# Kernel optimization log

Measured on AMD Instinct MI355X. Metric: run time of the kernel, lower is better.

Reference implementation:

```python
import jax, jax.numpy as jnp
import numpy as np

N, M, E0, E1, D, C_IN, NCLS = 100000, 10000, 1600000, 320000, 64, 4, 4


def setup_inputs() -> dict:
    key = jax.random.key(0)
    ks = jax.random.split(key, 16)
    w = lambda k, shp: jax.random.normal(k, shp, jnp.float32) * 0.05
    return {
        "features": jax.random.normal(ks[0], (N, C_IN), jnp.float32),
        "points": jax.random.uniform(ks[1], (N, 3), dtype=jnp.float32),
        "cluster_centers": jax.random.uniform(ks[2], (M, 3), dtype=jnp.float32),
        "labels": jax.random.randint(ks[3], (N,), 0, M, jnp.int32),
        "l0_edges": jax.random.randint(ks[4], (E0, 2), 0, N, jnp.int32),
        "l1_edges": jax.random.randint(ks[5], (E1, 2), 0, M, jnp.int32),
        "fe_W": w(ks[6], (C_IN + 3, D)), "fe_b": jnp.zeros((D,), jnp.float32),
        "gnn_Wh": w(ks[7], (3, D, 3)), "gnn_bh": jnp.zeros((3, 3), jnp.float32),
        "gnn_Wf": w(ks[8], (3, D + 3, D)), "gnn_bf": jnp.zeros((3, D), jnp.float32),
        "gnn_Wg": w(ks[9], (3, D, D)), "gnn_bg": jnp.zeros((3, D), jnp.float32),
        "m2l_W": w(ks[10], (D + 3, D)), "m2l_b": jnp.zeros((D,), jnp.float32),
        "l2m_W": w(ks[11], (D + 3, D)), "l2m_b": jnp.zeros((D,), jnp.float32),
        "cls_W1": w(ks[12], (D, D)), "cls_b1": jnp.zeros((D,), jnp.float32),
        "cls_W2": w(ks[13], (D, NCLS)), "cls_b2": jnp.zeros((NCLS,), jnp.float32),
    }


def _seg_max(x, idx, n):
    # unsorted segment max; empty segments -> 0 (TF scatter_max-with-floor style)
    agg = jax.ops.segment_max(x, idx, num_segments=n)
    return jnp.where(agg <= jnp.finfo(x.dtype).min * 0.5, 0.0, agg)


def _pointgnn_layer(x, pos, edges, Wh, bh, Wf, bf, Wg, bg):
    # PointGNN layer: offset MLP, edge MLP on gathered (rel_pos+offset, src feat),
    # scatter-max to destination, update MLP, residual.
    delta = jnp.tanh(x @ Wh + bh)                     # [n,3] learned coord offset
    s, d = edges[:, 0], edges[:, 1]
    rel = pos[s] - pos[d] + delta[d]                  # [E,3]
    e = jax.nn.relu(jnp.concatenate([rel, x[s]], -1) @ Wf + bf)  # [E,D]
    agg = _seg_max(e, d, x.shape[0])                  # [n,D]
    return jax.nn.relu(agg @ Wg + bg) + x


def _forward(features, points, cluster_centers, labels, l0_edges, l1_edges,
             fe_W, fe_b, gnn_Wh, gnn_bh, gnn_Wf, gnn_bf, gnn_Wg, gnn_bg,
             m2l_W, m2l_b, l2m_W, l2m_b, cls_W1, cls_b1, cls_W2, cls_b2):
    rel = points - cluster_centers[labels]            # [N,3] point rel to its center
    # layer1: Feature_extract
    x1 = jax.nn.relu(jnp.concatenate([features, rel], -1) @ fe_W + fe_b)
    # layer2: Mini_GNN on point graph
    x2 = _pointgnn_layer(x1, points, l0_edges, gnn_Wh[0], gnn_bh[0],
                         gnn_Wf[0], gnn_bf[0], gnn_Wg[0], gnn_bg[0])
    # layer3: Mini_to_Large (scatter-max pooling to clusters)
    h = jax.nn.relu(jnp.concatenate([x2, rel], -1) @ m2l_W + m2l_b)
    c = _seg_max(h, labels, cluster_centers.shape[0])  # [M,D]
    # layer4: GNN on cluster graph
    c4 = _pointgnn_layer(c, cluster_centers, l1_edges, gnn_Wh[1], gnn_bh[1],
                         gnn_Wf[1], gnn_bf[1], gnn_Wg[1], gnn_bg[1])
    # layer5: Large_to_Mini (broadcast cluster features back to points)
    x5 = jax.nn.relu(jnp.concatenate([c4[labels], rel], -1) @ l2m_W + l2m_b)
    # layer6: Mini_GNN on point graph
    x6 = _pointgnn_layer(x5, points, l0_edges, gnn_Wh[2], gnn_bh[2],
                         gnn_Wf[2], gnn_bf[2], gnn_Wg[2], gnn_bg[2])
    final = x6 + x2                                   # residual skip per source
    return jax.nn.relu(final @ cls_W1 + cls_b1) @ cls_W2 + cls_b2  # [N,NCLS]


def reference(features, points, cluster_centers, labels, l0_edges, l1_edges,
              fe_W, fe_b, gnn_Wh, gnn_bh, gnn_Wf, gnn_bf, gnn_Wg, gnn_bg,
              m2l_W, m2l_b, l2m_W, l2m_b, cls_W1, cls_b1, cls_W2, cls_b2):
    return _forward(features, points, cluster_centers, labels, l0_edges, l1_edges,
                    fe_W, fe_b, gnn_Wh, gnn_bh, gnn_Wf, gnn_bf, gnn_Wg, gnn_bg,
                    m2l_W, m2l_b, l2m_W, l2m_b, cls_W1, cls_b1, cls_W2, cls_b2)
```

## Files before the change

kernel.cpp:

```cpp
#include <hip/hip_runtime.h>


__device__ __forceinline__ float bcast(float v, int l) {
    return __int_as_float(__builtin_amdgcn_readlane(__float_as_int(v), l));
}

#define REPD(M,P,B) \
 M(0,P,B)  M(1,P,B)  M(2,P,B)  M(3,P,B)  M(4,P,B)  M(5,P,B)  M(6,P,B)  M(7,P,B) \
 M(8,P,B)  M(9,P,B)  M(10,P,B) M(11,P,B) M(12,P,B) M(13,P,B) M(14,P,B) M(15,P,B) \
 M(16,P,B) M(17,P,B) M(18,P,B) M(19,P,B) M(20,P,B) M(21,P,B) M(22,P,B) M(23,P,B) \
 M(24,P,B) M(25,P,B) M(26,P,B) M(27,P,B) M(28,P,B) M(29,P,B) M(30,P,B) M(31,P,B) \
 M(32,P,B) M(33,P,B) M(34,P,B) M(35,P,B) M(36,P,B) M(37,P,B) M(38,P,B) M(39,P,B) \
 M(40,P,B) M(41,P,B) M(42,P,B) M(43,P,B) M(44,P,B) M(45,P,B) M(46,P,B) M(47,P,B) \
 M(48,P,B) M(49,P,B) M(50,P,B) M(51,P,B) M(52,P,B) M(53,P,B) M(54,P,B) M(55,P,B) \
 M(56,P,B) M(57,P,B) M(58,P,B) M(59,P,B) M(60,P,B) M(61,P,B) M(62,P,B) M(63,P,B)

#define WLOAD(J,P,B) float P##J = (B)[(J)*64+lane];

#define REPP(M,P,X,S0,S1) \
 M(0,1,P,X,S0,S1)  M(2,3,P,X,S0,S1)  M(4,5,P,X,S0,S1)  M(6,7,P,X,S0,S1) \
 M(8,9,P,X,S0,S1)  M(10,11,P,X,S0,S1) M(12,13,P,X,S0,S1) M(14,15,P,X,S0,S1) \
 M(16,17,P,X,S0,S1) M(18,19,P,X,S0,S1) M(20,21,P,X,S0,S1) M(22,23,P,X,S0,S1) \
 M(24,25,P,X,S0,S1) M(26,27,P,X,S0,S1) M(28,29,P,X,S0,S1) M(30,31,P,X,S0,S1) \
 M(32,33,P,X,S0,S1) M(34,35,P,X,S0,S1) M(36,37,P,X,S0,S1) M(38,39,P,X,S0,S1) \
 M(40,41,P,X,S0,S1) M(42,43,P,X,S0,S1) M(44,45,P,X,S0,S1) M(46,47,P,X,S0,S1) \
 M(48,49,P,X,S0,S1) M(50,51,P,X,S0,S1) M(52,53,P,X,S0,S1) M(54,55,P,X,S0,S1) \
 M(56,57,P,X,S0,S1) M(58,59,P,X,S0,S1) M(60,61,P,X,S0,S1) M(62,63,P,X,S0,S1)

#define WFMA(J,K,P,X,S0,S1) \
 S0 = fmaf(bcast(X,J), P##J, S0); \
 S1 = fmaf(bcast(X,K), P##K, S1);


typedef short bf16x8 __attribute__((ext_vector_type(8)));
typedef float f32x4  __attribute__((ext_vector_type(4)));

__device__ __forceinline__ unsigned short f2bf_rne(float x) {
    unsigned u = __float_as_uint(x);
    unsigned r = u + 0x7FFFu + ((u >> 16) & 1u);
    return (unsigned short)(r >> 16);
}

__device__ __forceinline__ void a_frag(const float* __restrict__ row, int kt, int g4,
                                       bf16x8& ah, bf16x8& al)
{
    const float4 a0 = *(const float4*)(row + kt*32 + g4);
    const float4 a1 = *(const float4*)(row + kt*32 + 16 + g4);
    float v0 = a0.x, v1 = a0.y, v2 = a0.z, v3 = a0.w;
    float v4 = a1.x, v5 = a1.y, v6 = a1.z, v7 = a1.w;
#define CVT1(idx, val) { \
    unsigned short hh = f2bf_rne(val); \
    float lf = (val) - __uint_as_float((unsigned)hh << 16); \
    ah[idx] = (short)hh; al[idx] = (short)f2bf_rne(lf); }
    CVT1(0,v0) CVT1(1,v1) CVT1(2,v2) CVT1(3,v3)
    CVT1(4,v4) CVT1(5,v5) CVT1(6,v6) CVT1(7,v7)
#undef CVT1
}

__device__ __forceinline__ void mm64(const bf16x8& ah0, const bf16x8& al0,
                                     const bf16x8& ah1, const bf16x8& al1,
                                     const unsigned short* __restrict__ pW,
                                     int lane, f32x4 acc[4])
{
#pragma unroll
    for (int nt = 0; nt < 4; ++nt) {
        f32x4 a = {0.f, 0.f, 0.f, 0.f};
#pragma unroll
        for (int kt = 0; kt < 2; ++kt) {
            bf16x8 bh = *(const bf16x8*)(pW + (kt*4+nt)*1024 + lane*8);
            bf16x8 bl = *(const bf16x8*)(pW + (kt*4+nt)*1024 + 512 + lane*8);
            bf16x8 aH = kt ? ah1 : ah0;
            bf16x8 aL = kt ? al1 : al0;
            a = __builtin_amdgcn_mfma_f32_16x16x32_bf16(aH, bh, a, 0, 0, 0);
            a = __builtin_amdgcn_mfma_f32_16x16x32_bf16(aL, bh, a, 0, 0, 0);
            a = __builtin_amdgcn_mfma_f32_16x16x32_bf16(aH, bl, a, 0, 0, 0);
        }
        acc[nt] = a;
    }
}

__global__ __launch_bounds__(256) void k_packB7(
    const float* W0, unsigned short* d0, const float* W1, unsigned short* d1,
    const float* W2, unsigned short* d2, const float* W3, unsigned short* d3,
    const float* W4, unsigned short* d4, const float* W5, unsigned short* d5,
    const float* W6, unsigned short* d6)
{
    const float* W; unsigned short* dst;
    switch (blockIdx.x) {
        case 0: W=W0; dst=d0; break;
        case 1: W=W1; dst=d1; break;
        case 2: W=W2; dst=d2; break;
        case 3: W=W3; dst=d3; break;
        case 4: W=W4; dst=d4; break;
        case 5: W=W5; dst=d5; break;
        default: W=W6; dst=d6; break;
    }
    int t = threadIdx.x;
    for (int slot = t; slot < 512; slot += 256) {
        int frag = slot >> 6;
        int lane = slot & 63;
        int kt = frag >> 2, nt = frag & 3;
        int g4 = (lane >> 4) * 4, n = nt*16 + (lane & 15);
        for (int j = 0; j < 8; ++j) {
            int k = kt*32 + (j>>2)*16 + g4 + (j&3);
            float x = W[k*64 + n];
            unsigned short hh = f2bf_rne(x);
            float lf = x - __uint_as_float((unsigned)hh << 16);
            dst[frag*1024 + 0*512 + lane*8 + j] = hh;
            dst[frag*1024 + 1*512 + lane*8 + j] = f2bf_rne(lf);
        }
    }
}


__global__ __launch_bounds__(256) void k_zero3(
    int* c0, int n0, int* c1, int n1, int* c2, int n2)
{
    int t = threadIdx.x;
    for (int i = t; i < n0; i += 256) c0[i] = 0;
    for (int i = t; i < n1; i += 256) c1[i] = 0;
    for (int i = t; i < n2; i += 256) c2[i] = 0;
}

__global__ __launch_bounds__(256) void k_bhist3(
    const int2* __restrict__ e0, int* cnt0, int E0, int nb0,
    const int2* __restrict__ e1, int* cnt1, int E1, int nb1,
    const int* __restrict__ lab, int* cntL, int NN, int nbL)
{
    const int2* e = nullptr; const int* lv = nullptr; int* gcnt; int total; int nb;
    int bloc, nblocks;
    int b = blockIdx.x;
    if (b < 1024)      { e = e0; gcnt = cnt0; total = E0; nb = nb0; bloc = b;        nblocks = 1024; }
    else if (b < 1280) { e = e1; gcnt = cnt1; total = E1; nb = nb1; bloc = b - 1024; nblocks = 256; }
    else               { lv = lab; gcnt = cntL; total = NN; nb = nbL; bloc = b - 1280; nblocks = 256; }
    __shared__ int c[400];
    for (int i = threadIdx.x; i < nb; i += 256) c[i] = 0;
    __syncthreads();
    for (int idx = bloc*256 + threadIdx.x; idx < total; idx += nblocks*256)
        atomicAdd(&c[(lv ? lv[idx] : e[idx].y) >> 8], 1);
    __syncthreads();
    for (int i = threadIdx.x; i < nb; i += 256) if (c[i]) atomicAdd(&gcnt[i], c[i]);
}

__global__ __launch_bounds__(512) void k_bscan3(
    const int* c0, int* b0, int* u0, int nb0, int t0,
    const int* c1, int* b1, int* u1, int nb1, int t1,
    const int* c2, int* b2, int* u2, int nb2, int t2)
{
    const int* cnt; int* base; int* cur; int nb; int tot;
    if (blockIdx.x == 0) { cnt=c0; base=b0; cur=u0; nb=nb0; tot=t0; }
    else if (blockIdx.x == 1) { cnt=c1; base=b1; cur=u1; nb=nb1; tot=t1; }
    else { cnt=c2; base=b2; cur=u2; nb=nb2; tot=t2; }
    __shared__ int sc[512];
    int t = threadIdx.x;
    int v = (t < nb) ? cnt[t] : 0;
    sc[t] = v; __syncthreads();
    for (int o = 1; o < 512; o <<= 1) {
        int a = (t >= o) ? sc[t-o] : 0;
        __syncthreads();
        sc[t] += a;
        __syncthreads();
    }
    if (t < nb) { int ex = sc[t] - v; base[t] = ex; cur[t] = ex; }
    if (t == nb) base[nb] = tot;
}

#define BKT 512
#define EPT 8
#define EPB (BKT*EPT)
__global__ __launch_bounds__(BKT) void k_bucket3(
    const int2* __restrict__ e0, int* cur0, int2* eb0, int E0, int nb0, int GB0,
    const int2* __restrict__ e1, int* cur1, int2* eb1, int E1, int nb1, int GB1,
    const int* __restrict__ lab, int* curL, int2* ebL, int NN, int nbL)
{
    const int2* e = nullptr; const int* lv = nullptr; int* cur; int2* ebuf;
    int total; int nb; int bloc;
    int b = blockIdx.x;
    if (b < GB0)            { e = e0; cur = cur0; ebuf = eb0; total = E0; nb = nb0; bloc = b; }
    else if (b < GB0 + GB1) { e = e1; cur = cur1; ebuf = eb1; total = E1; nb = nb1; bloc = b - GB0; }
    else                    { lv = lab; cur = curL; ebuf = ebL; total = NN; nb = nbL; bloc = b - GB0 - GB1; }
    __shared__ int cnt[400];
    __shared__ int chunk[400];
    int t = threadIdx.x;
    int base = bloc * EPB;
    for (int i = t; i < nb; i += BKT) cnt[i] = 0;
    __syncthreads();
    int2 ed[EPT]; int rk[EPT];
#pragma unroll
    for (int k = 0; k < EPT; ++k) {
        int idx = base + k*BKT + t;
        if (idx < total) {
            ed[k] = lv ? make_int2(idx, lv[idx]) : e[idx];
            rk[k] = atomicAdd(&cnt[ed[k].y >> 8], 1);
        } else rk[k] = -1;
    }
    __syncthreads();
    for (int i = t; i < nb; i += BKT) { int c = cnt[i]; if (c) chunk[i] = atomicAdd(&cur[i], c); }
    __syncthreads();
#pragma unroll
    for (int k = 0; k < EPT; ++k)
        if (rk[k] >= 0) ebuf[chunk[ed[k].y >> 8] + rk[k]] = ed[k];
}

__global__ __launch_bounds__(512) void k_final3(
    const int2* eb0, const int* base0, int* rs0, int* srcs0, int nd0, int et0, int NB0_,
    const int2* eb1, const int* base1, int* rs1, int* srcs1, int nd1, int et1, int NB1_,
    const int2* ebL, const int* baseL, int* rsL, int* srcsL, int ndL, int etL, int NBL_)
{
    const int2* ebuf; const int* base_; int* rs; int* srcs; int ndst; int etot; int nb; int bloc;
    int b = blockIdx.x;
    if (b < NB0_)              { ebuf=eb0; base_=base0; rs=rs0; srcs=srcs0; ndst=nd0; etot=et0; nb=NB0_; bloc=b; }
    else if (b < NB0_ + NB1_)  { ebuf=eb1; base_=base1; rs=rs1; srcs=srcs1; ndst=nd1; etot=et1; nb=NB1_; bloc=b-NB0_; }
    else                       { ebuf=ebL; base_=baseL; rs=rsL; srcs=srcsL; ndst=ndL; etot=etL; nb=NBL_; bloc=b-NB0_-NB1_; }
    __shared__ int h[256];
    __shared__ int sc[256];
    int t = threadIdx.x;
    int base = base_[bloc];
    int cnt  = base_[bloc+1] - base;
    int d0 = bloc << 8;
    if (t < 256) h[t] = 0;
    __syncthreads();
    for (int i = t; i < cnt; i += 512) atomicAdd(&h[ebuf[base+i].y - d0], 1);
    __syncthreads();
    int v = (t < 256) ? h[t] : 0;
    if (t < 256) sc[t] = v;
    __syncthreads();
    for (int o = 1; o < 256; o <<= 1) {
        int a = (t < 256 && t >= o) ? sc[t-o] : 0;
        __syncthreads();
        if (t < 256) sc[t] += a;
        __syncthreads();
    }
    if (t < 256) {
        int gpos = base + sc[t] - v;
        if (d0 + t < ndst) rs[d0+t] = gpos;
        h[t] = gpos;
    }
    if (bloc == nb-1 && t == 0) rs[ndst] = etot;
    __syncthreads();
    for (int i = t; i < cnt; i += 512) {
        int2 ed = ebuf[base+i];
        int pos = atomicAdd(&h[ed.y - d0], 1);
        srcs[pos] = ed.x;
    }
}


__global__ __launch_bounds__(256) void k_feat_pre0_g(
    const float* __restrict__ feat, const float* __restrict__ pts,
    const float* __restrict__ ctr, const int* __restrict__ lab,
    const float* __restrict__ Wfe, const float* __restrict__ bfe,
    const float* __restrict__ Wh, const float* __restrict__ bh,
    const unsigned short* __restrict__ pWf0, const float* __restrict__ Wf0h,
    const float* __restrict__ bf0,
    float* __restrict__ rel, float* __restrict__ x1,
    float* __restrict__ p, float* __restrict__ q, int ntiles)
{
    __shared__ float xp[4][16*68];
    __shared__ float dd[4][64];
    int lane = threadIdx.x & 63;
    int w = threadIdx.x >> 6;
    int tile = blockIdx.x*4 + w;
    if (tile >= ntiles) return;
    int r0 = tile*16;
    int row = lane & 15;
    int cg  = lane >> 4;
    int r = r0 + row;
    int l = lab[r];
    float pr0 = pts[r*3+0], pr1 = pts[r*3+1], pr2 = pts[r*3+2];
    float rv0 = pr0 - ctr[l*3+0], rv1 = pr1 - ctr[l*3+1], rv2 = pr2 - ctr[l*3+2];
    if (cg == 0) { rel[r*3+0]=rv0; rel[r*3+1]=rv1; rel[r*3+2]=rv2; }
    float f0 = feat[r*4+0], f1 = feat[r*4+1], f2 = feat[r*4+2], f3 = feat[r*4+3];
#pragma unroll
    for (int k = 0; k < 16; ++k) {
        int c = cg*16 + k;
        float v = bfe[c];
        v = fmaf(f0, Wfe[0*64+c], v);
        v = fmaf(f1, Wfe[1*64+c], v);
        v = fmaf(f2, Wfe[2*64+c], v);
        v = fmaf(f3, Wfe[3*64+c], v);
        v = fmaf(rv0, Wfe[4*64+c], v);
        v = fmaf(rv1, Wfe[5*64+c], v);
        v = fmaf(rv2, Wfe[6*64+c], v);
        xp[w][row*68 + c] = fmaxf(v, 0.f);
    }
    {
        int j = cg < 3 ? cg : 2;
        float accd = 0.f;
#pragma unroll 16
        for (int k2 = 0; k2 < 64; ++k2)
            accd = fmaf(xp[w][row*68 + k2], Wh[k2*3 + j], accd);
        dd[w][row*4 + cg] = tanhf(accd + bh[j]);
    }
    int g4 = cg * 4;
    const float* lrow = &xp[w][row*68];
    bf16x8 ah0, al0, ah1, al1;
    a_frag(lrow, 0, g4, ah0, al0);
    a_frag(lrow, 1, g4, ah1, al1);
    f32x4 acc[4];
    mm64(ah0, al0, ah1, al1, pWf0, lane, acc);
    int rloc = cg*4;
#pragma unroll
    for (int nt = 0; nt < 4; ++nt) {
        int c = nt*16 + row;
        float w0t = Wf0h[0*64+c], w1t = Wf0h[1*64+c], w2t = Wf0h[2*64+c];
        float bfc = bf0[c];
#pragma unroll
        for (int reg = 0; reg < 4; ++reg) {
            int rr = r0 + rloc + reg;
            int rl = rloc + reg;
            float pp0 = pts[rr*3+0], pp1 = pts[rr*3+1], pp2 = pts[rr*3+2];
            float v = acc[nt][reg] + pp0*w0t + pp1*w1t + pp2*w2t;
            p[(size_t)rr*64 + c] = v;
            x1[(size_t)rr*64 + c] = xp[w][rl*68 + c];
            float d0 = dd[w][rl*4+0], d1 = dd[w][rl*4+1], d2 = dd[w][rl*4+2];
            q[(size_t)rr*64 + c] = (d0-pp0)*w0t + (d1-pp1)*w1t + (d2-pp2)*w2t + bfc;
        }
    }
}

__global__ __launch_bounds__(256) void k_post_m2l_g(
    const float* __restrict__ agg, const unsigned short* __restrict__ pWg,
    const float* __restrict__ bg, const float* __restrict__ x1,
    const unsigned short* __restrict__ pWm, const float* __restrict__ bm,
    const float* __restrict__ Wmt, const float* __restrict__ rel,
    float* __restrict__ x2, float* __restrict__ h, int ntiles)
{
    __shared__ float xp[4][16*68];
    int lane = threadIdx.x & 63;
    int w = threadIdx.x >> 6;
    int tile = blockIdx.x*4 + w;
    if (tile >= ntiles) return;
    int r0 = tile*16;
    int g4 = (lane >> 4) * 4;
    int rloc = (lane >> 4) * 4;
    const float* rowp = agg + (size_t)(r0 + (lane & 15)) * 64;
    bf16x8 ah0, al0, ah1, al1;
    a_frag(rowp, 0, g4, ah0, al0);
    a_frag(rowp, 1, g4, ah1, al1);
    f32x4 acc[4];
    mm64(ah0, al0, ah1, al1, pWg, lane, acc);
#pragma unroll
    for (int nt = 0; nt < 4; ++nt) {
        int c = nt*16 + (lane & 15);
        float bc = bg[c];
#pragma unroll
        for (int reg = 0; reg < 4; ++reg) {
            int r = r0 + rloc + reg;
            float v = fmaxf(acc[nt][reg] + bc, 0.f) + x1[(size_t)r*64 + c];
            x2[(size_t)r*64 + c] = v;
            xp[w][(rloc+reg)*68 + c] = v;
        }
    }
    const float* lrow = &xp[w][(lane & 15)*68];
    a_frag(lrow, 0, g4, ah0, al0);
    a_frag(lrow, 1, g4, ah1, al1);
    mm64(ah0, al0, ah1, al1, pWm, lane, acc);
#pragma unroll
    for (int nt = 0; nt < 4; ++nt) {
        int c = nt*16 + (lane & 15);
        float bc = bm[c];
        float w0t = Wmt[0*64+c], w1t = Wmt[1*64+c], w2t = Wmt[2*64+c];
#pragma unroll
        for (int reg = 0; reg < 4; ++reg) {
            int r = r0 + rloc + reg;
            float v = acc[nt][reg] + bc + rel[r*3+0]*w0t + rel[r*3+1]*w1t + rel[r*3+2]*w2t;
            h[(size_t)r*64 + c] = fmaxf(v, 0.f);
        }
    }
}

__global__ __launch_bounds__(256) void k_l2m_pre2_g(
    const float* __restrict__ c4, const int* __restrict__ lab,
    const unsigned short* __restrict__ pWl, const float* __restrict__ bl,
    const float* __restrict__ Wlt, const float* __restrict__ rel,
    const unsigned short* __restrict__ pWf2, const float* __restrict__ Wf2t,
    const float* __restrict__ pts,
    const float* __restrict__ Wh, const float* __restrict__ bh,
    const float* __restrict__ bf,
    float* __restrict__ x5, float* __restrict__ p, float* __restrict__ q, int ntiles)
{
    __shared__ float xp[4][16*68];
    __shared__ float dd[4][64];
    int lane = threadIdx.x & 63;
    int w = threadIdx.x >> 6;
    int tile = blockIdx.x*4 + w;
    if (tile >= ntiles) return;
    int r0 = tile*16;
    int g4 = (lane >> 4) * 4;
    int rloc = (lane >> 4) * 4;
    int rA = r0 + (lane & 15);
    const float* rowp = c4 + (size_t)lab[rA] * 64;
    bf16x8 ah0, al0, ah1, al1;
    a_frag(rowp, 0, g4, ah0, al0);
    a_frag(rowp, 1, g4, ah1, al1);
    f32x4 acc[4];
    mm64(ah0, al0, ah1, al1, pWl, lane, acc);
#pragma unroll
    for (int nt = 0; nt < 4; ++nt) {
        int c = nt*16 + (lane & 15);
        float bc = bl[c];
        float w0t = Wlt[0*64+c], w1t = Wlt[1*64+c], w2t = Wlt[2*64+c];
#pragma unroll
        for (int reg = 0; reg < 4; ++reg) {
            int r = r0 + rloc + reg;
            float v = acc[nt][reg] + bc + rel[r*3+0]*w0t + rel[r*3+1]*w1t + rel[r*3+2]*w2t;
            v = fmaxf(v, 0.f);
            x5[(size_t)r*64 + c] = v;
            xp[w][(rloc+reg)*68 + c] = v;
        }
    }
    {
        int rowl = lane & 15;
        int jj = lane >> 4;
        int j = jj < 3 ? jj : 2;
        float accd = 0.f;
#pragma unroll 16
        for (int k = 0; k < 64; ++k)
            accd = fmaf(xp[w][rowl*68 + k], Wh[k*3 + j], accd);
        dd[w][rowl*4 + jj] = tanhf(accd + bh[j]);
    }
    const float* lrow = &xp[w][(lane & 15)*68];
    a_frag(lrow, 0, g4, ah0, al0);
    a_frag(lrow, 1, g4, ah1, al1);
    mm64(ah0, al0, ah1, al1, pWf2, lane, acc);
#pragma unroll
    for (int nt = 0; nt < 4; ++nt) {
        int c = nt*16 + (lane & 15);
        float w0t = Wf2t[0*64+c], w1t = Wf2t[1*64+c], w2t = Wf2t[2*64+c];
        float bfc = bf[c];
#pragma unroll
        for (int reg = 0; reg < 4; ++reg) {
            int r = r0 + rloc + reg;
            int rl = rloc + reg;
            float p0 = pts[r*3+0], p1 = pts[r*3+1], p2 = pts[r*3+2];
            float v = acc[nt][reg] + p0*w0t + p1*w1t + p2*w2t;
            p[(size_t)r*64 + c] = v;
            float d0 = dd[w][rl*4+0], d1 = dd[w][rl*4+1], d2 = dd[w][rl*4+2];
            q[(size_t)r*64 + c] = (d0-p0)*w0t + (d1-p1)*w1t + (d2-p2)*w2t + bfc;
        }
    }
}

__global__ __launch_bounds__(256) void k_gemm_final(
    const float* __restrict__ agg, const unsigned short* __restrict__ pWg2,
    const float* __restrict__ bg2,
    const float* __restrict__ x5, const float* __restrict__ x2,
    const unsigned short* __restrict__ pW1, const float* __restrict__ b1,
    const float* __restrict__ W2, const float* __restrict__ b2,
    float* __restrict__ out, int ntiles)
{
    __shared__ float xp[4][16*68];
    int lane = threadIdx.x & 63;
    int w = threadIdx.x >> 6;
    int tile = blockIdx.x*4 + w;
    if (tile >= ntiles) return;
    int r0 = tile*16;
    int g4 = (lane >> 4) * 4;
    int rloc = (lane >> 4) * 4;
    const float* rowp = agg + (size_t)(r0 + (lane & 15)) * 64;
    bf16x8 ah0, al0, ah1, al1;
    a_frag(rowp, 0, g4, ah0, al0);
    a_frag(rowp, 1, g4, ah1, al1);
    f32x4 acc[4];
    mm64(ah0, al0, ah1, al1, pWg2, lane, acc);
#pragma unroll
    for (int nt = 0; nt < 4; ++nt) {
        int c = nt*16 + (lane & 15);
        float bc = bg2[c];
#pragma unroll
        for (int reg = 0; reg < 4; ++reg) {
            int r = r0 + rloc + reg;
            float v = fmaxf(acc[nt][reg] + bc, 0.f)
                    + x5[(size_t)r*64 + c] + x2[(size_t)r*64 + c];
            xp[w][(rloc+reg)*68 + c] = v;
        }
    }
    const float* lrow = &xp[w][(lane & 15)*68];
    a_frag(lrow, 0, g4, ah0, al0);
    a_frag(lrow, 1, g4, ah1, al1);
    mm64(ah0, al0, ah1, al1, pW1, lane, acc);
    float part0[4] = {0.f,0.f,0.f,0.f};
    float part1[4] = {0.f,0.f,0.f,0.f};
    float part2[4] = {0.f,0.f,0.f,0.f};
    float part3[4] = {0.f,0.f,0.f,0.f};
#pragma unroll
    for (int nt = 0; nt < 4; ++nt) {
        int c = nt*16 + (lane & 15);
        float bc = b1[c];
        float4 w2v = *(const float4*)(W2 + c*4);
#pragma unroll
        for (int reg = 0; reg < 4; ++reg) {
            float t = fmaxf(acc[nt][reg] + bc, 0.f);
            part0[reg] = fmaf(t, w2v.x, part0[reg]);
            part1[reg] = fmaf(t, w2v.y, part1[reg]);
            part2[reg] = fmaf(t, w2v.z, part2[reg]);
            part3[reg] = fmaf(t, w2v.w, part3[reg]);
        }
    }
#pragma unroll
    for (int m = 1; m < 16; m <<= 1) {
#pragma unroll
        for (int reg = 0; reg < 4; ++reg) {
            part0[reg] += __shfl_xor(part0[reg], m);
            part1[reg] += __shfl_xor(part1[reg], m);
            part2[reg] += __shfl_xor(part2[reg], m);
            part3[reg] += __shfl_xor(part3[reg], m);
        }
    }
    if ((lane & 15) == 0) {
        float b20 = b2[0], b21 = b2[1], b22 = b2[2], b23 = b2[3];
#pragma unroll
        for (int reg = 0; reg < 4; ++reg) {
            int r = r0 + rloc + reg;
            *(float4*)(out + (size_t)r*4) =
                make_float4(part0[reg]+b20, part1[reg]+b21, part2[reg]+b22, part3[reg]+b23);
        }
    }
}


__global__ __launch_bounds__(256) void k_seg_max_gnn(
    const int* __restrict__ rs, const int* __restrict__ srcs,
    const float* __restrict__ p, float* __restrict__ q, int n)
{
    int lane = threadIdx.x & 63;
    int wid  = blockIdx.x * (blockDim.x >> 6) + (threadIdx.x >> 6);
    int nw   = gridDim.x * (blockDim.x >> 6);
    for (int d0 = wid*2; d0 < n; d0 += nw*2) {
        int dA = __builtin_amdgcn_readfirstlane(d0);
        int begA = rs[dA], endA = rs[dA+1], endB = rs[dA+2];
        int ca = begA, cb = endA;
        float aA[8], aB[8];
#pragma unroll
        for (int u = 0; u < 8; ++u) { aA[u] = -1e30f; aB[u] = -1e30f; }
        while (ca+8 <= endA && cb+8 <= endB) {
            int sA[8], sB[8];
#pragma unroll
            for (int u = 0; u < 8; ++u) { sA[u] = srcs[ca+u]; sB[u] = srcs[cb+u]; }
#pragma unroll
            for (int u = 0; u < 8; ++u) {
                aA[u] = fmaxf(aA[u], p[(size_t)sA[u]*64+lane]);
                aB[u] = fmaxf(aB[u], p[(size_t)sB[u]*64+lane]);
            }
            ca += 8; cb += 8;
        }
        while (ca+4 <= endA) {
            int s0=srcs[ca], s1=srcs[ca+1], s2=srcs[ca+2], s3=srcs[ca+3];
            aA[0] = fmaxf(aA[0], p[(size_t)s0*64+lane]);
            aA[1] = fmaxf(aA[1], p[(size_t)s1*64+lane]);
            aA[2] = fmaxf(aA[2], p[(size_t)s2*64+lane]);
            aA[3] = fmaxf(aA[3], p[(size_t)s3*64+lane]);
            ca += 4;
        }
        while (cb+4 <= endB) {
            int t0=srcs[cb], t1=srcs[cb+1], t2=srcs[cb+2], t3=srcs[cb+3];
            aB[0] = fmaxf(aB[0], p[(size_t)t0*64+lane]);
            aB[1] = fmaxf(aB[1], p[(size_t)t1*64+lane]);
            aB[2] = fmaxf(aB[2], p[(size_t)t2*64+lane]);
            aB[3] = fmaxf(aB[3], p[(size_t)t3*64+lane]);
            cb += 4;
        }
        while (ca+2 <= endA) {
            int s0=srcs[ca], s1=srcs[ca+1];
            aA[0] = fmaxf(aA[0], p[(size_t)s0*64+lane]);
            aA[1] = fmaxf(aA[1], p[(size_t)s1*64+lane]);
            ca += 2;
        }
        while (cb+2 <= endB) {
            int t0=srcs[cb], t1=srcs[cb+1];
            aB[0] = fmaxf(aB[0], p[(size_t)t0*64+lane]);
            aB[1] = fmaxf(aB[1], p[(size_t)t1*64+lane]);
            cb += 2;
        }
        if (ca < endA) aA[0] = fmaxf(aA[0], p[(size_t)srcs[ca]*64+lane]);
        if (cb < endB) aB[0] = fmaxf(aB[0], p[(size_t)srcs[cb]*64+lane]);
        float accA = fmaxf(fmaxf(fmaxf(aA[0],aA[1]), fmaxf(aA[2],aA[3])),
                           fmaxf(fmaxf(aA[4],aA[5]), fmaxf(aA[6],aA[7])));
        float accB = fmaxf(fmaxf(fmaxf(aB[0],aB[1]), fmaxf(aB[2],aB[3])),
                           fmaxf(fmaxf(aB[4],aB[5]), fmaxf(aB[6],aB[7])));
        size_t oA = (size_t)dA*64 + lane, oB = oA + 64;
        q[oA] = fmaxf(accA + q[oA], 0.f);
        q[oB] = fmaxf(accB + q[oB], 0.f);
    }
}

__global__ __launch_bounds__(256, 2) void k_seglab_pre1(
    const int* __restrict__ rsL, const int* __restrict__ srcsL,
    const float* __restrict__ h, const float* __restrict__ pos,
    const float* __restrict__ Wh, const float* __restrict__ bh,
    const float* __restrict__ Wf, const float* __restrict__ bf,
    float* __restrict__ c, float* __restrict__ pa, float* __restrict__ qa, int m)
{
    int lane = threadIdx.x & 63;
    int wid  = blockIdx.x * (blockDim.x >> 6) + (threadIdx.x >> 6);
    int nw   = gridDim.x * (blockDim.x >> 6);
    REPD(WLOAD, wc, Wf + 3*64)
    float w0 = Wf[0*64+lane], w1 = Wf[1*64+lane], w2 = Wf[2*64+lane];
    float bfl = bf[lane];
    float wh0 = Wh[lane*3+0], wh1 = Wh[lane*3+1], wh2 = Wh[lane*3+2];
    float bh0 = bh[0], bh1 = bh[1], bh2 = bh[2];
    for (int d0 = wid*2; d0 < m; d0 += nw*2) {
        int dA = __builtin_amdgcn_readfirstlane(d0);
        int dB = dA + 1;
        int begA = rsL[dA], endA = rsL[dA+1], endB = rsL[dA+2];
        int ca = begA, cb = endA;
        float aA0=-1e30f, aA1=-1e30f, aB0=-1e30f, aB1=-1e30f;
        while (ca+2 <= endA && cb+2 <= endB) {
            int s0=srcsL[ca], s1=srcsL[ca+1], s2=srcsL[cb], s3=srcsL[cb+1];
            aA0 = fmaxf(aA0, h[(size_t)s0*64+lane]);
            aA1 = fmaxf(aA1, h[(size_t)s1*64+lane]);
            aB0 = fmaxf(aB0, h[(size_t)s2*64+lane]);
            aB1 = fmaxf(aB1, h[(size_t)s3*64+lane]);
            ca += 2; cb += 2;
        }
        while (ca+2 <= endA) {
            int s0=srcsL[ca], s1=srcsL[ca+1];
            aA0 = fmaxf(aA0, h[(size_t)s0*64+lane]);
            aA1 = fmaxf(aA1, h[(size_t)s1*64+lane]);
            ca += 2;
        }
        while (cb+2 <= endB) {
            int s2=srcsL[cb], s3=srcsL[cb+1];
            aB0 = fmaxf(aB0, h[(size_t)s2*64+lane]);
            aB1 = fmaxf(aB1, h[(size_t)s3*64+lane]);
            cb += 2;
        }
        if (ca < endA) aA0 = fmaxf(aA0, h[(size_t)srcsL[ca]*64+lane]);
        if (cb < endB) aB0 = fmaxf(aB0, h[(size_t)srcsL[cb]*64+lane]);
        float cvA = fmaxf(fmaxf(aA0,aA1), 0.f);
        float cvB = fmaxf(fmaxf(aB0,aB1), 0.f);
        c[(size_t)dA*64+lane] = cvA;
        c[(size_t)dB*64+lane] = cvB;
        float d0A = cvA*wh0, d1A = cvA*wh1, d2A = cvA*wh2;
        float d0B = cvB*wh0, d1B = cvB*wh1, d2B = cvB*wh2;
#pragma unroll
        for (int o = 32; o; o >>= 1) {
            d0A += __shfl_xor(d0A,o); d1A += __shfl_xor(d1A,o); d2A += __shfl_xor(d2A,o);
            d0B += __shfl_xor(d0B,o); d1B += __shfl_xor(d1B,o); d2B += __shfl_xor(d2B,o);
        }
        d0A = tanhf(d0A+bh0); d1A = tanhf(d1A+bh1); d2A = tanhf(d2A+bh2);
        d0B = tanhf(d0B+bh0); d1B = tanhf(d1B+bh1); d2B = tanhf(d2B+bh2);
        float pA0 = pos[dA*3+0], pA1 = pos[dA*3+1], pA2 = pos[dA*3+2];
        float pB0 = pos[dB*3+0], pB1 = pos[dB*3+1], pB2 = pos[dB*3+2];
        float s0A=0.f, s1A=0.f, s0B=0.f, s1B=0.f;
        REPP(WFMA, wc, cvA, s0A, s1A)
        REPP(WFMA, wc, cvB, s0B, s1B)
        pa[(size_t)dA*64+lane] = s0A+s1A + pA0*w0 + pA1*w1 + pA2*w2;
        pa[(size_t)dB*64+lane] = s0B+s1B + pB0*w0 + pB1*w1 + pB2*w2;
        qa[(size_t)dA*64+lane] = (d0A-pA0)*w0 + (d1A-pA1)*w1 + (d2A-pA2)*w2 + bfl;
        qa[(size_t)dB*64+lane] = (d0B-pB0)*w0 + (d1B-pB1)*w1 + (d2B-pB2)*w2 + bfl;
    }
}

__global__ __launch_bounds__(256, 2) void k_gnn_post(
    const float* __restrict__ agg, const float* __restrict__ Wg,
    const float* __restrict__ bg, const float* __restrict__ xres,
    float* __restrict__ out, int n)
{
    int lane = threadIdx.x & 63;
    int wid  = blockIdx.x * (blockDim.x >> 6) + (threadIdx.x >> 6);
    int nw   = gridDim.x * (blockDim.x >> 6);
    REPD(WLOAD, wg, Wg)
    float bgl = bg[lane];
    for (int i0 = wid*2; i0 < n; i0 += nw*2) {
        int iA = __builtin_amdgcn_readfirstlane(i0);
        size_t oA = (size_t)iA*64 + lane, oB = oA + 64;
        float avA = agg[oA], avB = agg[oB];
        float s0A=0.f, s1A=0.f, s0B=0.f, s1B=0.f;
        REPP(WFMA, wg, avA, s0A, s1A)
        REPP(WFMA, wg, avB, s0B, s1B)
        out[oA] = fmaxf(s0A+s1A + bgl, 0.f) + xres[oA];
        out[oB] = fmaxf(s0B+s1B + bgl, 0.f) + xres[oB];
    }
}


extern "C" void kernel_launch(void* const* d_in, const int* in_sizes, int n_in,
                              void* d_out, int out_size, void* d_ws, size_t ws_size,
                              hipStream_t stream)
{
    const int N = 100000, M = 10000, E0 = 1600000, E1 = 320000;
    const int NB0 = (N + 255) / 256;
    const int NB1 = (M + 255) / 256;
    const int NBL = (M + 255) / 256;
    const int GB0 = (E0 + EPB - 1) / EPB;
    const int GB1 = (E1 + EPB - 1) / EPB;
    const int GBL = (N + EPB - 1) / EPB;

    const float* feat = (const float*)d_in[0];
    const float* pts  = (const float*)d_in[1];
    const float* ctr  = (const float*)d_in[2];
    const int*   lab  = (const int*)d_in[3];
    const int2*  e0   = (const int2*)d_in[4];
    const int2*  e1   = (const int2*)d_in[5];
    const float* feW  = (const float*)d_in[6];
    const float* feb  = (const float*)d_in[7];
    const float* Wh   = (const float*)d_in[8];
    const float* bh   = (const float*)d_in[9];
    const float* Wf   = (const float*)d_in[10];
    const float* bf   = (const float*)d_in[11];
    const float* Wg   = (const float*)d_in[12];
    const float* bg   = (const float*)d_in[13];
    const float* m2lW = (const float*)d_in[14];
    const float* m2lb = (const float*)d_in[15];
    const float* l2mW = (const float*)d_in[16];
    const float* l2mb = (const float*)d_in[17];
    const float* cW1  = (const float*)d_in[18];
    const float* cb1  = (const float*)d_in[19];
    const float* cW2  = (const float*)d_in[20];
    const float* cb2  = (const float*)d_in[21];
    float* out = (float*)d_out;

    char* ws = (char*)d_ws;
    size_t off = 0;
    auto alloc = [&](size_t bytes) -> char* {
        char* r = ws + off; off += (bytes + 255) & ~(size_t)255; return r;
    };
    float* rel   = (float*)alloc((size_t)N*3*4);
    float* x1    = (float*)alloc((size_t)N*64*4);
    float* x2    = (float*)alloc((size_t)N*64*4);
    float* p     = (float*)alloc((size_t)N*64*4);
    float* q     = (float*)alloc((size_t)N*64*4);
    float* c     = (float*)alloc((size_t)M*64*4);
    float* c4    = (float*)alloc((size_t)M*64*4);
    int* rs0     = (int*)alloc((size_t)(N+2)*4);
    int* srcs0   = (int*)alloc((size_t)E0*4);
    int* rs1     = (int*)alloc((size_t)(M+2)*4);
    int* srcs1   = (int*)alloc((size_t)E1*4);
    int* rsL     = (int*)alloc((size_t)(M+2)*4);
    int* srcsL   = (int*)alloc((size_t)N*4);
    int* cnt0    = (int*)alloc((size_t)NB0*4);
    int* cnt1    = (int*)alloc((size_t)NB1*4);
    int* cntL    = (int*)alloc((size_t)NBL*4);
    int* base0   = (int*)alloc((size_t)(NB0+1)*4);
    int* base1   = (int*)alloc((size_t)(NB1+1)*4);
    int* baseL   = (int*)alloc((size_t)(NBL+1)*4);
    int* cur0    = (int*)alloc((size_t)NB0*4);
    int* cur1    = (int*)alloc((size_t)NB1*4);
    int* curL    = (int*)alloc((size_t)NBL*4);
    unsigned short* pWf0  = (unsigned short*)alloc(8192*2);
    unsigned short* pWg0  = (unsigned short*)alloc(8192*2);
    unsigned short* pWm   = (unsigned short*)alloc(8192*2);
    unsigned short* pWl2m = (unsigned short*)alloc(8192*2);
    unsigned short* pWf2  = (unsigned short*)alloc(8192*2);
    unsigned short* pWg2  = (unsigned short*)alloc(8192*2);
    unsigned short* pW1   = (unsigned short*)alloc(8192*2);
    (void)ws_size; (void)in_sizes; (void)n_in; (void)out_size;

    int2* ebuf0 = (int2*)x2;
    int2* ebuf1 = ebuf0 + E0;
    int2* ebufL = ebuf1 + E1;

    dim3 blk(256);
    const int gridM = 640, gSeg = 3072;
    const int NT = N / 16;
    const int gG = (NT + 3) / 4;

    k_packB7<<<7, blk, 0, stream>>>(
        Wf + 0*67*64 + 3*64, pWf0,
        Wg + 0*64*64,        pWg0,
        m2lW,                pWm,
        l2mW,                pWl2m,
        Wf + 2*67*64 + 3*64, pWf2,
        Wg + 2*64*64,        pWg2,
        cW1,                 pW1);

    k_zero3<<<1, blk, 0, stream>>>(cnt0, NB0, cnt1, NB1, cntL, NBL);
    k_bhist3<<<1536, blk, 0, stream>>>(e0, cnt0, E0, NB0,
                                       e1, cnt1, E1, NB1,
                                       lab, cntL, N, NBL);
    k_bscan3<<<3, 512, 0, stream>>>(cnt0, base0, cur0, NB0, E0,
                                    cnt1, base1, cur1, NB1, E1,
                                    cntL, baseL, curL, NBL, N);
    k_bucket3<<<GB0 + GB1 + GBL, BKT, 0, stream>>>(
        e0, cur0, ebuf0, E0, NB0, GB0,
        e1, cur1, ebuf1, E1, NB1, GB1,
        lab, curL, ebufL, N, NBL);
    k_final3<<<NB0 + NB1 + NBL, 512, 0, stream>>>(
        ebuf0, base0, rs0, srcs0, N, E0, NB0,
        ebuf1, base1, rs1, srcs1, M, E1, NB1,
        ebufL, baseL, rsL, srcsL, M, N, NBL);

    k_feat_pre0_g<<<gG, blk, 0, stream>>>(feat, pts, ctr, lab, feW, feb,
                                          Wh+0*64*3, bh+0*3,
                                          pWf0, Wf+0*67*64, bf+0*64,
                                          rel, x1, p, q, NT);
    k_seg_max_gnn<<<gSeg, blk, 0, stream>>>(rs0, srcs0, p, q, N);
    k_post_m2l_g<<<gG, blk, 0, stream>>>(q, pWg0, bg+0*64, x1,
                                         pWm, m2lb, m2lW+64*64, rel,
                                         x2, p, NT);

    float* p1 = q;
    float* q1 = q + (size_t)M*64;
    k_seglab_pre1<<<gridM, blk, 0, stream>>>(rsL, srcsL, p, ctr,
                                             Wh+1*64*3, bh+1*3, Wf+1*67*64, bf+1*64,
                                             c, p1, q1, M);
    k_seg_max_gnn<<<640, blk, 0, stream>>>(rs1, srcs1, p1, q1, M);
    k_gnn_post<<<gridM, blk, 0, stream>>>(q1, Wg+1*64*64, bg+1*64, c, c4, M);

    k_l2m_pre2_g<<<gG, blk, 0, stream>>>(c4, lab, pWl2m, l2mb, l2mW+64*64, rel,
                                         pWf2, Wf+2*67*64, pts,
                                         Wh+2*64*3, bh+2*3, bf+2*64,
                                         x1, p, q, NT);
    k_seg_max_gnn<<<gSeg, blk, 0, stream>>>(rs0, srcs0, p, q, N);
    k_gemm_final<<<gG, blk, 0, stream>>>(q, pWg2, bg+2*64, x1, x2,
                                         pW1, cb1, cW2, cb2, out, NT);
}
```

Measured before the change: 333.4 us.

## Fuse weight packing with histogram kernel and rewrite segment-max gather as float2 half-waves

The weight-packing kernel and the edge/label histogram kernel are merged into one launch, which removes one kernel launch. The seg-max kernel now handles one destination per wave instead of two. Each half-wave gathers alternating source rows with float2 loads, and the two halves are combined with a cross-lane shuffle. The aim is wider per-lane loads and more independent gathers in flight, at the cost of an extra shuffle. The seg-max grid also shrinks from 3072 to 2048 blocks.

```diff
diff --git a/kernel.cpp b/kernel.cpp
--- a/kernel.cpp
+++ b/kernel.cpp
@@ -79,39 +79,66 @@
     }
 }
 
-__global__ __launch_bounds__(256) void k_packB7(
+
+#define BKT 512
+#define EPT 8
+#define EPB (BKT*EPT)
+
+__global__ __launch_bounds__(256) void k_prep(
     const float* W0, unsigned short* d0, const float* W1, unsigned short* d1,
     const float* W2, unsigned short* d2, const float* W3, unsigned short* d3,
     const float* W4, unsigned short* d4, const float* W5, unsigned short* d5,
-    const float* W6, unsigned short* d6)
-{
-    const float* W; unsigned short* dst;
-    switch (blockIdx.x) {
-        case 0: W=W0; dst=d0; break;
-        case 1: W=W1; dst=d1; break;
-        case 2: W=W2; dst=d2; break;
-        case 3: W=W3; dst=d3; break;
-        case 4: W=W4; dst=d4; break;
-        case 5: W=W5; dst=d5; break;
-        default: W=W6; dst=d6; break;
-    }
-    int t = threadIdx.x;
-    for (int slot = t; slot < 512; slot += 256) {
-        int frag = slot >> 6;
-        int lane = slot & 63;
-        int kt = frag >> 2, nt = frag & 3;
-        int g4 = (lane >> 4) * 4, n = nt*16 + (lane & 15);
-        for (int j = 0; j < 8; ++j) {
-            int k = kt*32 + (j>>2)*16 + g4 + (j&3);
-            float x = W[k*64 + n];
-            unsigned short hh = f2bf_rne(x);
-            float lf = x - __uint_as_float((unsigned)hh << 16);
-            dst[frag*1024 + 0*512 + lane*8 + j] = hh;
-            dst[frag*1024 + 1*512 + lane*8 + j] = f2bf_rne(lf);
-        }
-    }
-}
-
+    const float* W6, unsigned short* d6,
+    int* cnt0, int nb0, int* cnt1, int nb1, int* cntL, int nbL,
+    const int2* __restrict__ e0, int E0,
+    const int2* __restrict__ e1, int E1,
+    const int* __restrict__ lab, int NN)
+{
+    int b = blockIdx.x;
+    if (b < 7) {
+        const float* W; unsigned short* dst;
+        switch (b) {
+            case 0: W=W0; dst=d0; break;
+            case 1: W=W1; dst=d1; break;
+            case 2: W=W2; dst=d2; break;
+            case 3: W=W3; dst=d3; break;
+            case 4: W=W4; dst=d4; break;
+            case 5: W=W5; dst=d5; break;
+            default: W=W6; dst=d6; break;
+        }
+        int t = threadIdx.x;
+        for (int slot = t; slot < 512; slot += 256) {
+            int frag = slot >> 6;
+            int lane = slot & 63;
+            int kt = frag >> 2, nt = frag & 3;
+            int g4 = (lane >> 4) * 4, n = nt*16 + (lane & 15);
+            for (int j = 0; j < 8; ++j) {
+                int k = kt*32 + (j>>2)*16 + g4 + (j&3);
+                float x = W[k*64 + n];
+                unsigned short hh = f2bf_rne(x);
+                float lf = x - __uint_as_float((unsigned)hh << 16);
+                dst[frag*1024 + 0*512 + lane*8 + j] = hh;
+                dst[frag*1024 + 1*512 + lane*8 + j] = f2bf_rne(lf);
+            }
+        }
+        return;
+    }
+    {
+        const int2* e = nullptr; const int* lv = nullptr; int* gcnt; int total; int nb;
+        int bloc, nblocks;
+        int bb = b - 7;
+        if (bb < 1024)      { e = e0; gcnt = cnt0; total = E0; nb = nb0; bloc = bb;        nblocks = 1024; }
+        else if (bb < 1280) { e = e1; gcnt = cnt1; total = E1; nb = nb1; bloc = bb - 1024; nblocks = 256; }
+        else                { lv = lab; gcnt = cntL; total = NN; nb = nbL; bloc = bb - 1280; nblocks = 256; }
+        __shared__ int c[400];
+        for (int i = threadIdx.x; i < nb; i += 256) c[i] = 0;
+        __syncthreads();
+        for (int idx = bloc*256 + threadIdx.x; idx < total; idx += nblocks*256)
+            atomicAdd(&c[(lv ? lv[idx] : e[idx].y) >> 8], 1);
+        __syncthreads();
+        for (int i = threadIdx.x; i < nb; i += 256) if (c[i]) atomicAdd(&gcnt[i], c[i]);
+    }
+}
 
 __global__ __launch_bounds__(256) void k_zero3(
     int* c0, int n0, int* c1, int n1, int* c2, int n2)
@@ -120,26 +147,6 @@
     for (int i = t; i < n0; i += 256) c0[i] = 0;
     for (int i = t; i < n1; i += 256) c1[i] = 0;
     for (int i = t; i < n2; i += 256) c2[i] = 0;
-}
-
-__global__ __launch_bounds__(256) void k_bhist3(
-    const int2* __restrict__ e0, int* cnt0, int E0, int nb0,
-    const int2* __restrict__ e1, int* cnt1, int E1, int nb1,
-    const int* __restrict__ lab, int* cntL, int NN, int nbL)
-{
-    const int2* e = nullptr; const int* lv = nullptr; int* gcnt; int total; int nb;
-    int bloc, nblocks;
-    int b = blockIdx.x;
-    if (b < 1024)      { e = e0; gcnt = cnt0; total = E0; nb = nb0; bloc = b;        nblocks = 1024; }
-    else if (b < 1280) { e = e1; gcnt = cnt1; total = E1; nb = nb1; bloc = b - 1024; nblocks = 256; }
-    else               { lv = lab; gcnt = cntL; total = NN; nb = nbL; bloc = b - 1280; nblocks = 256; }
-    __shared__ int c[400];
-    for (int i = threadIdx.x; i < nb; i += 256) c[i] = 0;
-    __syncthreads();
-    for (int idx = bloc*256 + threadIdx.x; idx < total; idx += nblocks*256)
-        atomicAdd(&c[(lv ? lv[idx] : e[idx].y) >> 8], 1);
-    __syncthreads();
-    for (int i = threadIdx.x; i < nb; i += 256) if (c[i]) atomicAdd(&gcnt[i], c[i]);
 }
 
 __global__ __launch_bounds__(512) void k_bscan3(
@@ -165,9 +172,6 @@
     if (t == nb) base[nb] = tot;
 }
 
-#define BKT 512
-#define EPT 8
-#define EPB (BKT*EPT)
 __global__ __launch_bounds__(BKT) void k_bucket3(
     const int2* __restrict__ e0, int* cur0, int2* eb0, int E0, int nb0, int GB0,
     const int2* __restrict__ e1, int* cur1, int2* eb1, int E1, int nb1, int GB1,
@@ -525,63 +529,68 @@
     const float* __restrict__ p, float* __restrict__ q, int n)
 {
     int lane = threadIdx.x & 63;
+    int half = lane >> 5;
+    int cl   = lane & 31;
     int wid  = blockIdx.x * (blockDim.x >> 6) + (threadIdx.x >> 6);
     int nw   = gridDim.x * (blockDim.x >> 6);
-    for (int d0 = wid*2; d0 < n; d0 += nw*2) {
-        int dA = __builtin_amdgcn_readfirstlane(d0);
-        int begA = rs[dA], endA = rs[dA+1], endB = rs[dA+2];
-        int ca = begA, cb = endA;
-        float aA[8], aB[8];
-#pragma unroll
-        for (int u = 0; u < 8; ++u) { aA[u] = -1e30f; aB[u] = -1e30f; }
-        while (ca+8 <= endA && cb+8 <= endB) {
-            int sA[8], sB[8];
-#pragma unroll
-            for (int u = 0; u < 8; ++u) { sA[u] = srcs[ca+u]; sB[u] = srcs[cb+u]; }
+    const float2* p2 = (const float2*)p;
+    for (int d = wid; d < n; d += nw) {
+        int du = __builtin_amdgcn_readfirstlane(d);
+        int beg = rs[du], end = rs[du+1];
+        float ax[8], ay[8];
+#pragma unroll
+        for (int u = 0; u < 8; ++u) { ax[u] = -1e30f; ay[u] = -1e30f; }
+        int c = beg;
+        while (c + 16 <= end) {
+            int s[8];
+#pragma unroll
+            for (int u = 0; u < 8; ++u) s[u] = srcs[c + 2*u + half];
 #pragma unroll
             for (int u = 0; u < 8; ++u) {
-                aA[u] = fmaxf(aA[u], p[(size_t)sA[u]*64+lane]);
-                aB[u] = fmaxf(aB[u], p[(size_t)sB[u]*64+lane]);
+                float2 v = p2[(size_t)s[u]*32 + cl];
+                ax[u] = fmaxf(ax[u], v.x);
+                ay[u] = fmaxf(ay[u], v.y);
             }
-            ca += 8; cb += 8;
-        }
-        while (ca+4 <= endA) {
-            int s0=srcs[ca], s1=srcs[ca+1], s2=srcs[ca+2], s3=srcs[ca+3];
-            aA[0] = fmaxf(aA[0], p[(size_t)s0*64+lane]);
-            aA[1] = fmaxf(aA[1], p[(size_t)s1*64+lane]);
-            aA[2] = fmaxf(aA[2], p[(size_t)s2*64+lane]);
-            aA[3] = fmaxf(aA[3], p[(size_t)s3*64+lane]);
-            ca += 4;
-        }
-        while (cb+4 <= endB) {
-            int t0=srcs[cb], t1=srcs[cb+1], t2=srcs[cb+2], t3=srcs[cb+3];
-            aB[0] = fmaxf(aB[0], p[(size_t)t0*64+lane]);
-            aB[1] = fmaxf(aB[1], p[(size_t)t1*64+lane]);
-            aB[2] = fmaxf(aB[2], p[(size_t)t2*64+lane]);
-            aB[3] = fmaxf(aB[3], p[(size_t)t3*64+lane]);
-            cb += 4;
-        }
-        while (ca+2 <= endA) {
-            int s0=srcs[ca], s1=srcs[ca+1];
-            aA[0] = fmaxf(aA[0], p[(size_t)s0*64+lane]);
-            aA[1] = fmaxf(aA[1], p[(size_t)s1*64+lane]);
-            ca += 2;
-        }
-        while (cb+2 <= endB) {
-            int t0=srcs[cb], t1=srcs[cb+1];
-            aB[0] = fmaxf(aB[0], p[(size_t)t0*64+lane]);
-            aB[1] = fmaxf(aB[1], p[(size_t)t1*64+lane]);
-            cb += 2;
-        }
-        if (ca < endA) aA[0] = fmaxf(aA[0], p[(size_t)srcs[ca]*64+lane]);
-        if (cb < endB) aB[0] = fmaxf(aB[0], p[(size_t)srcs[cb]*64+lane]);
-        float accA = fmaxf(fmaxf(fmaxf(aA[0],aA[1]), fmaxf(aA[2],aA[3])),
-                           fmaxf(fmaxf(aA[4],aA[5]), fmaxf(aA[6],aA[7])));
-        float accB = fmaxf(fmaxf(fmaxf(aB[0],aB[1]), fmaxf(aB[2],aB[3])),
-                           fmaxf(fmaxf(aB[4],aB[5]), fmaxf(aB[6],aB[7])));
-        size_t oA = (size_t)dA*64 + lane, oB = oA + 64;
-        q[oA] = fmaxf(accA + q[oA], 0.f);
-        q[oB] = fmaxf(accB + q[oB], 0.f);
+            c += 16;
+        }
+        while (c + 8 <= end) {
+            int s0 = srcs[c + half],     s1 = srcs[c + 2 + half];
+            int s2 = srcs[c + 4 + half], s3 = srcs[c + 6 + half];
+            float2 v0 = p2[(size_t)s0*32 + cl];
+            float2 v1 = p2[(size_t)s1*32 + cl];
+            float2 v2 = p2[(size_t)s2*32 + cl];
+            float2 v3 = p2[(size_t)s3*32 + cl];
+            ax[0] = fmaxf(ax[0], v0.x); ay[0] = fmaxf(ay[0], v0.y);
+            ax[1] = fmaxf(ax[1], v1.x); ay[1] = fmaxf(ay[1], v1.y);
+            ax[2] = fmaxf(ax[2], v2.x); ay[2] = fmaxf(ay[2], v2.y);
+            ax[3] = fmaxf(ax[3], v3.x); ay[3] = fmaxf(ay[3], v3.y);
+            c += 8;
+        }
+        while (c + 2 <= end) {
+            int s0 = srcs[c + half];
+            float2 v = p2[(size_t)s0*32 + cl];
+            ax[0] = fmaxf(ax[0], v.x);
+            ay[0] = fmaxf(ay[0], v.y);
+            c += 2;
+        }
+        if (c < end) {
+            int s0 = srcs[c];
+            float2 v = p2[(size_t)s0*32 + cl];
+            ax[0] = fmaxf(ax[0], v.x);
+            ay[0] = fmaxf(ay[0], v.y);
+        }
+        float mx = fmaxf(fmaxf(fmaxf(ax[0],ax[1]), fmaxf(ax[2],ax[3])),
+                         fmaxf(fmaxf(ax[4],ax[5]), fmaxf(ax[6],ax[7])));
+        float my = fmaxf(fmaxf(fmaxf(ay[0],ay[1]), fmaxf(ay[2],ay[3])),
+                         fmaxf(fmaxf(ay[4],ay[5]), fmaxf(ay[6],ay[7])));
+        mx = fmaxf(mx, __shfl_xor(mx, 32));
+        my = fmaxf(my, __shfl_xor(my, 32));
+        if (half == 0) {
+            float2* q2 = (float2*)q;
+            size_t o = (size_t)du*32 + cl;
+            float2 qv = q2[o];
+            q2[o] = make_float2(fmaxf(mx + qv.x, 0.f), fmaxf(my + qv.y, 0.f));
+        }
     }
 }
 
@@ -753,23 +762,21 @@
     int2* ebufL = ebuf1 + E1;
 
     dim3 blk(256);
-    const int gridM = 640, gSeg = 3072;
+    const int gridM = 640, gSeg = 2048;
     const int NT = N / 16;
     const int gG = (NT + 3) / 4;
 
-    k_packB7<<<7, blk, 0, stream>>>(
+    k_zero3<<<1, blk, 0, stream>>>(cnt0, NB0, cnt1, NB1, cntL, NBL);
+    k_prep<<<7 + 1536, blk, 0, stream>>>(
         Wf + 0*67*64 + 3*64, pWf0,
         Wg + 0*64*64,        pWg0,
         m2lW,                pWm,
         l2mW,                pWl2m,
         Wf + 2*67*64 + 3*64, pWf2,
         Wg + 2*64*64,        pWg2,
-        cW1,                 pW1);
-
-    k_zero3<<<1, blk, 0, stream>>>(cnt0, NB0, cnt1, NB1, cntL, NBL);
-    k_bhist3<<<1536, blk, 0, stream>>>(e0, cnt0, E0, NB0,
-                                       e1, cnt1, E1, NB1,
-                                       lab, cntL, N, NBL);
+        cW1,                 pW1,
+        cnt0, NB0, cnt1, NB1, cntL, NBL,
+        e0, E0, e1, E1, lab, N);
     k_bscan3<<<3, 512, 0, stream>>>(cnt0, base0, cur0, NB0, E0,
                                     cnt1, base1, cur1, NB1, E1,
                                     cntL, baseL, curL, NBL, N);
```

Measured after the change: 336.7 us. About the same (+1.0%).
